# Performance work log

Hardware: AMD Instinct MI355X
Metric: run time of the kernel (lower is better)

Reference implementation:

```python
import jax, jax.numpy as jnp
import numpy as np

EMBED_DIM = 1024
NUM_HEADS = 16
HEAD_DIM = EMBED_DIM // NUM_HEADS
EXPANSION = 4
EPS = 1e-5


def setup_inputs() -> dict:
    key = jax.random.key(0)
    ks = jax.random.split(key, 8)
    D, F = EMBED_DIM, EMBED_DIM * EXPANSION
    s = lambda d: 1.0 / np.sqrt(d)
    return {
        "x": jax.random.normal(ks[0], (8, 1024, D), jnp.float32),
        "qkv_w": jax.random.normal(ks[1], (D, 3 * D), jnp.float32) * s(D),
        "qkv_b": jnp.zeros((3 * D,), jnp.float32),
        "out_w": jax.random.normal(ks[2], (D, D), jnp.float32) * s(D),
        "out_b": jnp.zeros((D,), jnp.float32),
        "ffn_w1": jax.random.normal(ks[3], (D, F), jnp.float32) * s(D),
        "ffn_b1": jnp.zeros((F,), jnp.float32),
        "ffn_w2": jax.random.normal(ks[4], (F, D), jnp.float32) * s(F),
        "ffn_b2": jnp.zeros((D,), jnp.float32),
        "ln1_g": jnp.ones((D,), jnp.float32),
        "ln1_b": jnp.zeros((D,), jnp.float32),
        "ln2_g": jnp.ones((D,), jnp.float32),
        "ln2_b": jnp.zeros((D,), jnp.float32),
    }


def _layernorm(x, g, b):
    mu = jnp.mean(x, axis=-1, keepdims=True)
    var = jnp.mean(jnp.square(x - mu), axis=-1, keepdims=True)
    return (x - mu) * jax.lax.rsqrt(var + EPS) * g + b


def reference(x, qkv_w, qkv_b, out_w, out_b, ffn_w1, ffn_b1, ffn_w2, ffn_b2,
              ln1_g, ln1_b, ln2_g, ln2_b):
    B, N, D = x.shape
    H, Hd = NUM_HEADS, HEAD_DIM
    scale = Hd ** -0.5

    residual = x
    h = _layernorm(x, ln1_g, ln1_b)
    qkv = h @ qkv_w + qkv_b                      # [B, N, 3D]
    q, k, v = jnp.split(qkv, 3, axis=-1)
    # [B, N, D] -> [B, H, N, Hd]
    reshape = lambda t: t.reshape(B, N, H, Hd).transpose(0, 2, 1, 3)
    q, k, v = reshape(q), reshape(k), reshape(v)

    attn = jnp.einsum("bhnd,bhmd->bhnm", q, k) * scale
    attn = jax.nn.softmax(attn, axis=-1)
    o = jnp.einsum("bhnm,bhmd->bhnd", attn, v)   # [B, H, N, Hd]
    o = o.transpose(0, 2, 1, 3).reshape(B, N, D)
    o = o @ out_w + out_b
    x = residual + o

    residual = x
    h = _layernorm(x, ln2_g, ln2_b)
    h = jax.nn.gelu(h @ ffn_w1 + ffn_b1, approximate=False) @ ffn_w2 + ffn_b2
    return residual + h
```

## Files before the change

kernel.cpp:

```cpp
#include <hip/hip_runtime.h>
#include <hip/hip_bf16.h>


typedef float f32x4 __attribute__((ext_vector_type(4)));
typedef float f32x16 __attribute__((ext_vector_type(16)));
typedef short bf16x8 __attribute__((ext_vector_type(8)));

#define DEV __device__ __forceinline__

DEV f32x4 mfma16(bf16x8 a, bf16x8 b, f32x4 c) {
    return __builtin_amdgcn_mfma_f32_16x16x32_bf16(a, b, c, 0, 0, 0);
}

DEV f32x16 mfma32(bf16x8 a, bf16x8 b, f32x16 c) {
    return __builtin_amdgcn_mfma_f32_32x32x16_bf16(a, b, c, 0, 0, 0);
}

DEV ushort f2bf(float f) {
    union { float f; unsigned u; } v; v.f = f;
    unsigned r = v.u + 0x7FFFu + ((v.u >> 16) & 1u);
    return (ushort)(r >> 16);
}

DEV unsigned cvtpk(float lo, float hi) {
    unsigned r;
    asm("v_cvt_pk_bf16_f32 %0, %1, %2" : "=v"(r) : "v"(lo), "v"(hi));
    return r;
}

DEV void gload_lds16(const void* g, void* l) {
    __builtin_amdgcn_global_load_lds(
        (const __attribute__((address_space(1))) void*)g,
        (__attribute__((address_space(3))) void*)l, 16, 0, 0);
}

template <int N> DEV void vmw() {
    if constexpr (N == 0)      asm volatile("s_waitcnt vmcnt(0)" ::: "memory");
    else if constexpr (N == 3) asm volatile("s_waitcnt vmcnt(3)" ::: "memory");
    else if constexpr (N == 4) asm volatile("s_waitcnt vmcnt(4)" ::: "memory");
    __builtin_amdgcn_sched_barrier(0);
}

#define SBAR() do { __builtin_amdgcn_sched_barrier(0); \
                    __builtin_amdgcn_s_barrier(); \
                    __builtin_amdgcn_sched_barrier(0); } while (0)
#define LGKM0() do { asm volatile("s_waitcnt lgkmcnt(0)" ::: "memory"); \
                     __builtin_amdgcn_sched_barrier(0); } while (0)

__global__ __launch_bounds__(256) void transpose_w(
    const float* __restrict__ src, ushort* __restrict__ dst, int K, int N)
{
    __shared__ float tile[32][33];
    const int n0 = blockIdx.x * 32, k0 = blockIdx.y * 32;
    const int tx = threadIdx.x, ty = threadIdx.y;
#pragma unroll
    for (int i = 0; i < 32; i += 8)
        tile[ty + i][tx] = src[(size_t)(k0 + ty + i) * N + n0 + tx];
    __syncthreads();
#pragma unroll
    for (int i = 0; i < 32; i += 8)
        dst[(size_t)(n0 + ty + i) * K + k0 + tx] = f2bf(tile[tx][ty + i]);
}

__global__ __launch_bounds__(256) void transpose_v(
    const ushort* __restrict__ qkvb, ushort* __restrict__ vt)
{
    __shared__ ushort tile[32][33];
    const int b = blockIdx.z >> 4, h = blockIdx.z & 15;
    const int n0 = blockIdx.x * 32, d0 = blockIdx.y * 32;
    const int tx = threadIdx.x, ty = threadIdx.y;
#pragma unroll
    for (int i = 0; i < 32; i += 8)
        tile[ty + i][tx] =
            qkvb[(size_t)(b * 1024 + n0 + ty + i) * 3072 + 2048 + h * 64 + d0 + tx];
    __syncthreads();
#pragma unroll
    for (int i = 0; i < 32; i += 8)
        vt[((size_t)(b * 16 + h) * 64 + d0 + ty + i) * 1024 + n0 + tx] = tile[tx][ty + i];
}

__global__ __launch_bounds__(256) void ln_bf16(
    const float* __restrict__ x, const float* __restrict__ gw,
    const float* __restrict__ bw, ushort* __restrict__ out)
{
    const int row = blockIdx.x;
    const int t = threadIdx.x;
    const float4 v = ((const float4*)(x + (size_t)row * 1024))[t];
    float s  = v.x + v.y + v.z + v.w;
    float s2 = v.x * v.x + v.y * v.y + v.z * v.z + v.w * v.w;
#pragma unroll
    for (int off = 32; off; off >>= 1) {
        s  += __shfl_xor(s, off);
        s2 += __shfl_xor(s2, off);
    }
    __shared__ float red[16];
    const int wave = t >> 6, lane = t & 63;
    if (lane == 0) { red[wave] = s; red[8 + wave] = s2; }
    __syncthreads();
    s  = red[0] + red[1] + red[2] + red[3];
    s2 = red[8] + red[9] + red[10] + red[11];
    const float mean = s * (1.0f / 1024.0f);
    const float var  = s2 * (1.0f / 1024.0f) - mean * mean;
    const float rstd = rsqrtf(var + 1e-5f);
    const float4 gv = ((const float4*)gw)[t];
    const float4 bv = ((const float4*)bw)[t];
    ushort4 o;
    o.x = f2bf((v.x - mean) * rstd * gv.x + bv.x);
    o.y = f2bf((v.y - mean) * rstd * gv.y + bv.y);
    o.z = f2bf((v.z - mean) * rstd * gv.z + bv.z);
    o.w = f2bf((v.w - mean) * rstd * gv.w + bv.w);
    ((ushort4*)out)[(size_t)row * 256 + t] = o;
}

template <int BM, int BN, int WM_, int WN_, int EPI>
__global__ __launch_bounds__(512, 2) void gemm8p(
    const ushort* __restrict__ A, const ushort* __restrict__ BT,
    const float* __restrict__ bias, const float* __restrict__ res,
    void* __restrict__ out, int M, int N, int K)
{
    constexpr int BK = 64;
    constexpr int MR = BM / WM_ / 16;
    constexpr int NR = BN / WN_ / 16;
    constexpr int MQ = MR / 2, NQ = NR / 2;
    constexpr int LA = (BM / 2) * BK * 2 / (512 * 16);
    constexpr int LB = (BN / 2) * BK * 2 / (512 * 16);
    constexpr int VMN = LA + LB;
    constexpr int ABYTES = BM * BK * 2;
    constexpr int BBYTES = BN * BK * 2;

    extern __shared__ __align__(16) char smem[];
#define ASB(buf) (smem + (buf) * ABYTES)
#define BSB(buf) (smem + 2 * ABYTES + (buf) * BBYTES)

    const int tid = threadIdx.x;
    const int wave = tid >> 6, lane = tid & 63;
    const int g = lane >> 4, lr = lane & 15;
    const int wr = wave / WN_, wc = wave % WN_;
    const int akey = (lr & 7) << 4;

    const int gx = gridDim.x;
    const int nwg = gx * gridDim.y;
    int id = blockIdx.y * gx + blockIdx.x;
    id = (id & 7) * (nwg >> 3) + (id >> 3);
    const int m0 = (id / gx) * BM, n0 = (id % gx) * BN;

    const int trow = tid >> 3;
    const int tblk = (tid & 7) ^ (trow & 7);
    const ushort* pA = A  + (size_t)(m0 + trow) * K + tblk * 8;
    const ushort* pB = BT + (size_t)(n0 + trow) * K + tblk * 8;
    const int woff = wave * 1024;

#define STAGE_A(buf, mh, kt) do { \
    _Pragma("unroll") for (int i = 0; i < LA; ++i) \
        gload_lds16(pA + ((size_t)((mh) * (BM / 2) + i * 64)) * K + (kt) * 64, \
                    ASB(buf) + (mh) * (BM / 2) * 128 + i * 8192 + woff); \
} while (0)
#define STAGE_B(buf, nh, kt) do { \
    _Pragma("unroll") for (int i = 0; i < LB; ++i) \
        gload_lds16(pB + ((size_t)((nh) * (BN / 2) + i * 64)) * K + (kt) * 64, \
                    BSB(buf) + (nh) * (BN / 2) * 128 + i * 8192 + woff); \
} while (0)

    bf16x8 af[MQ][2], bf[NR][2];
    f32x4 acc[MR][NR] = {};

#define LOAD_A(buf, mh) do { \
    const char* hb_ = ASB(buf) + (mh) * (BM / 2) * 128 + (wr * (MQ * 16) + lr) * 128; \
    _Pragma("unroll") for (int mt = 0; mt < MQ; ++mt) \
    _Pragma("unroll") for (int kk = 0; kk < 2; ++kk) \
        af[mt][kk] = *(const bf16x8*)(hb_ + mt * 2048 + ((kk * 64 + g * 16) ^ akey)); \
} while (0)
#define LOAD_B(buf, nh) do { \
    const char* hb_ = BSB(buf) + (nh) * (BN / 2) * 128 + (wc * (NQ * 16) + lr) * 128; \
    _Pragma("unroll") for (int nt = 0; nt < NQ; ++nt) \
    _Pragma("unroll") for (int kk = 0; kk < 2; ++kk) \
        bf[(nh) * NQ + nt][kk] = *(const bf16x8*)(hb_ + nt * 2048 + ((kk * 64 + g * 16) ^ akey)); \
} while (0)
#define MFMA_Q(MH, NH) do { \
    __builtin_amdgcn_s_setprio(1); \
    _Pragma("unroll") for (int mt = 0; mt < MQ; ++mt) \
    _Pragma("unroll") for (int nt = 0; nt < NQ; ++nt) \
    _Pragma("unroll") for (int kk = 0; kk < 2; ++kk) \
        acc[(MH) * MQ + mt][(NH) * NQ + nt] = \
            mfma16(af[mt][kk], bf[(NH) * NQ + nt][kk], acc[(MH) * MQ + mt][(NH) * NQ + nt]); \
    __builtin_amdgcn_s_setprio(0); \
} while (0)

    const int NT = K >> 6;

    STAGE_A(0, 0, 0); STAGE_B(0, 0, 0); STAGE_B(0, 1, 0); STAGE_A(0, 1, 0);
    STAGE_A(1, 0, 1); STAGE_B(1, 0, 1);
    vmw<VMN>();
    __builtin_amdgcn_s_barrier();

    for (int kt = 0; kt < NT; ++kt) {
        const int buf = kt & 1, nbuf = buf ^ 1;
        LOAD_A(buf, 0); LOAD_B(buf, 0);
        if (kt + 1 < NT) STAGE_B(nbuf, 1, kt + 1);
        SBAR(); LGKM0(); MFMA_Q(0, 0); SBAR();
        LOAD_B(buf, 1);
        if (kt + 1 < NT) STAGE_A(nbuf, 1, kt + 1);
        SBAR(); LGKM0(); MFMA_Q(0, 1); SBAR();
        LOAD_A(buf, 1);
        if (kt + 2 < NT) STAGE_A(buf, 0, kt + 2);
        SBAR(); LGKM0(); MFMA_Q(1, 1); SBAR();
        if (kt + 2 < NT) STAGE_B(buf, 0, kt + 2);
        SBAR(); LGKM0(); MFMA_Q(1, 0);
        if (kt + 2 < NT)      vmw<VMN>();
        else if (kt + 1 < NT) vmw<0>();
        SBAR();
    }

#pragma unroll
    for (int mi = 0; mi < MR; ++mi) {
        const int row0 = m0 + (mi / MQ) * (BM / 2) + wr * (MQ * 16) + (mi % MQ) * 16 + 4 * g;
#pragma unroll
        for (int ni = 0; ni < NR; ++ni) {
            const int col = n0 + (ni / NQ) * (BN / 2) + wc * (NQ * 16) + (ni % NQ) * 16 + lr;
            const float bv = bias[col];
#pragma unroll
            for (int r = 0; r < 4; ++r) {
                float v = acc[mi][ni][r] + bv;
                const size_t idx = (size_t)(row0 + r) * N + col;
                if constexpr (EPI == 1) {
                    ((float*)out)[idx] = v + res[idx];
                } else if constexpr (EPI == 2) {
                    v = 0.5f * v * (1.0f + erff(v * 0.70710678118654752f));
                    ((ushort*)out)[idx] = f2bf(v);
                } else {
                    ((ushort*)out)[idx] = f2bf(v);
                }
            }
        }
    }
#undef STAGE_A
#undef STAGE_B
#undef LOAD_A
#undef LOAD_B
#undef MFMA_Q
#undef ASB
#undef BSB
}

__global__ __launch_bounds__(256) void attn_kernel(
    const ushort* __restrict__ qkv, const ushort* __restrict__ vtb,
    ushort* __restrict__ o)
{
    __shared__ __align__(16) ushort Ks[64 * 64];
    __shared__ __align__(16) ushort Vt[64 * 64];

    const int tid = threadIdx.x;
    const int wave = tid >> 6, lane = tid & 63;
    const int lq = lane & 31;
    const int hi = lane >> 5;
    const int l7 = lane & 7;

    const int hwid = blockIdx.x;
    const int logical = (hwid & 7) * 128 + (hwid >> 3);
    const int bh = logical >> 3, qt = logical & 7;
    const int b = bh >> 4, head = bh & 15;
    const int q0 = qt * 128 + wave * 32;

    const size_t base  = (size_t)b * 1024 * 3072;
    const size_t vbase = (size_t)bh * 64 * 1024;

    union BF8 { bf16x8 v; ushort u[8]; unsigned w[4]; };

    BF8 qf[4];
    {
        const ushort* qrow = qkv + base + (size_t)(q0 + lq) * 3072 + head * 64;
#pragma unroll
        for (int s = 0; s < 4; ++s) {
            *(ushort4*)&qf[s].u[0] = *(const ushort4*)(qrow + 16 * s + 4 * hi);
            *(ushort4*)&qf[s].u[4] = *(const ushort4*)(qrow + 16 * s + 8 + 4 * hi);
        }
    }

    const int sr = tid >> 3, sc = tid & 7;
    const int swz = (sc ^ (sr & 7)) << 3;
    const ushort* kg0 = qkv + base + (size_t)sr * 3072 + 1024 + head * 64 + sc * 8;
    const ushort* kg1 = kg0 + (size_t)32 * 3072;
    const ushort* vg0 = vtb + vbase + (size_t)sr * 1024 + sc * 8;
    const ushort* vg1 = vg0 + (size_t)32 * 1024;
    ushort* ksw0 = Ks + sr * 64 + swz;
    ushort* ksw1 = Ks + (sr + 32) * 64 + swz;
    ushort* vsw0 = Vt + sr * 64 + swz;
    ushort* vsw1 = Vt + (sr + 32) * 64 + swz;

    float m_st = -1e30f, l_st = 0.f;
    f32x16 oacc[2] = {};

    constexpr float SCL = 0.18033688011112042f;

    for (int kt = 0; kt < 16; ++kt) {
        const int n0 = kt * 64;
        __syncthreads();
        *(bf16x8*)ksw0 = *(const bf16x8*)(kg0 + (size_t)n0 * 3072);
        *(bf16x8*)ksw1 = *(const bf16x8*)(kg1 + (size_t)n0 * 3072);
        *(bf16x8*)vsw0 = *(const bf16x8*)(vg0 + n0);
        *(bf16x8*)vsw1 = *(const bf16x8*)(vg1 + n0);
        __syncthreads();

        f32x16 sacc[2];
#pragma unroll
        for (int kb = 0; kb < 2; ++kb) {
            f32x16 a = {};
            const ushort* krow = Ks + (kb * 32 + lq) * 64;
#pragma unroll
            for (int s = 0; s < 4; ++s) {
                BF8 kf;
                *(ushort4*)&kf.u[0] = *(const ushort4*)(krow + (((2 * s)     ^ l7) << 3) + 4 * hi);
                *(ushort4*)&kf.u[4] = *(const ushort4*)(krow + (((2 * s + 1) ^ l7) << 3) + 4 * hi);
                a = mfma32(kf.v, qf[s].v, a);
            }
            sacc[kb] = a;
        }

        float mloc = -1e30f;
#pragma unroll
        for (int kb = 0; kb < 2; ++kb)
#pragma unroll
            for (int r = 0; r < 16; ++r)
                mloc = fmaxf(mloc, sacc[kb][r]);
        mloc = fmaxf(mloc, __shfl_xor(mloc, 32));
        const float mnew = fmaxf(m_st, mloc * SCL);
        const float resc = exp2f(m_st - mnew);
        m_st = mnew;

        float psum = 0.f;
#pragma unroll
        for (int kb = 0; kb < 2; ++kb)
#pragma unroll
            for (int r = 0; r < 16; ++r) {
                const float pe = exp2f(fmaf(sacc[kb][r], SCL, -mnew));
                sacc[kb][r] = pe;
                psum += pe;
            }
        psum += __shfl_xor(psum, 32);
        l_st = l_st * resc + psum;
#pragma unroll
        for (int nb = 0; nb < 2; ++nb)
#pragma unroll
            for (int r = 0; r < 16; ++r)
                oacc[nb][r] *= resc;

#pragma unroll
        for (int kb = 0; kb < 2; ++kb) {
            BF8 pf[2];
#pragma unroll
            for (int t = 0; t < 2; ++t)
#pragma unroll
                for (int w = 0; w < 4; ++w)
                    pf[t].w[w] = cvtpk(sacc[kb][8 * t + 2 * w], sacc[kb][8 * t + 2 * w + 1]);
#pragma unroll
            for (int nb = 0; nb < 2; ++nb) {
                const ushort* vrow = Vt + (nb * 32 + lq) * 64;
#pragma unroll
                for (int t = 0; t < 2; ++t) {
                    BF8 vf;
                    const int blk = 4 * kb + 2 * t;
                    *(ushort4*)&vf.u[0] = *(const ushort4*)(vrow + ((blk       ^ l7) << 3) + 4 * hi);
                    *(ushort4*)&vf.u[4] = *(const ushort4*)(vrow + (((blk + 1) ^ l7) << 3) + 4 * hi);
                    oacc[nb] = mfma32(vf.v, pf[t].v, oacc[nb]);
                }
            }
        }
    }

    const float inv = 1.0f / l_st;
    ushort* orow = o + (size_t)(b * 1024 + q0 + lq) * 1024 + head * 64;
#pragma unroll
    for (int nb = 0; nb < 2; ++nb)
#pragma unroll
        for (int u = 0; u < 4; ++u) {
            uint2 wv;
            wv.x = cvtpk(oacc[nb][4 * u] * inv,     oacc[nb][4 * u + 1] * inv);
            wv.y = cvtpk(oacc[nb][4 * u + 2] * inv, oacc[nb][4 * u + 3] * inv);
            *(uint2*)(orow + nb * 32 + 8 * u + 4 * hi) = wv;
        }
}

extern "C" void kernel_launch(void* const* d_in, const int* in_sizes, int n_in,
                              void* d_out, int out_size, void* d_ws, size_t ws_size,
                              hipStream_t stream)
{
    const float* x      = (const float*)d_in[0];
    const float* qkv_w  = (const float*)d_in[1];
    const float* qkv_b  = (const float*)d_in[2];
    const float* out_w  = (const float*)d_in[3];
    const float* out_b  = (const float*)d_in[4];
    const float* ffn_w1 = (const float*)d_in[5];
    const float* ffn_b1 = (const float*)d_in[6];
    const float* ffn_w2 = (const float*)d_in[7];
    const float* ffn_b2 = (const float*)d_in[8];
    const float* ln1_g  = (const float*)d_in[9];
    const float* ln1_b  = (const float*)d_in[10];
    const float* ln2_g  = (const float*)d_in[11];
    const float* ln2_b  = (const float*)d_in[12];

    constexpr size_t MB = 1u << 20;
    char* ws = (char*)d_ws;
    ushort* wt_qkv = (ushort*)(ws + 0 * MB);
    ushort* wt_out = (ushort*)(ws + 6 * MB);
    ushort* wt_f1  = (ushort*)(ws + 8 * MB);
    ushort* wt_f2  = (ushort*)(ws + 16 * MB);
    float*  x1     = (float*) (ws + 24 * MB);
    ushort* vtb    = (ushort*)(ws + 24 * MB);
    ushort* hbuf   = (ushort*)(ws + 56 * MB);
    ushort* qkvb   = (ushort*)(ws + 72 * MB);
    ushort* obuf   = (ushort*)(ws + 120 * MB);
    ushort* gbuf   = (ushort*)(ws + 72 * MB);

    const dim3 tb(32, 8);
    transpose_w<<<dim3(3072 / 32, 1024 / 32), tb, 0, stream>>>(qkv_w,  wt_qkv, 1024, 3072);
    transpose_w<<<dim3(1024 / 32, 1024 / 32), tb, 0, stream>>>(out_w,  wt_out, 1024, 1024);
    transpose_w<<<dim3(4096 / 32, 1024 / 32), tb, 0, stream>>>(ffn_w1, wt_f1,  1024, 4096);
    transpose_w<<<dim3(1024 / 32, 4096 / 32), tb, 0, stream>>>(ffn_w2, wt_f2,  4096, 1024);

    ln_bf16<<<8192, 256, 0, stream>>>(x, ln1_g, ln1_b, hbuf);

    constexpr int LDS_256 = (256 * 64 * 2 + 256 * 64 * 2) * 2;
    constexpr int LDS_128 = (256 * 64 * 2 + 128 * 64 * 2) * 2;

    gemm8p<256, 256, 2, 4, 0><<<dim3(12, 32), 512, LDS_256, stream>>>(
        hbuf, wt_qkv, qkv_b, nullptr, qkvb, 8192, 3072, 1024);

    transpose_v<<<dim3(32, 2, 128), tb, 0, stream>>>(qkvb, vtb);

    attn_kernel<<<1024, 256, 0, stream>>>(qkvb, vtb, obuf);

    gemm8p<256, 128, 4, 2, 1><<<dim3(8, 32), 512, LDS_128, stream>>>(
        obuf, wt_out, out_b, x, x1, 8192, 1024, 1024);

    ln_bf16<<<8192, 256, 0, stream>>>(x1, ln2_g, ln2_b, hbuf);

    gemm8p<256, 256, 2, 4, 2><<<dim3(16, 32), 512, LDS_256, stream>>>(
        hbuf, wt_f1, ffn_b1, nullptr, gbuf, 8192, 4096, 1024);

    gemm8p<256, 128, 4, 2, 1><<<dim3(8, 32), 512, LDS_128, stream>>>(
        gbuf, wt_f2, ffn_b2, x1, (float*)d_out, 8192, 1024, 4096);
}
```

Before: 388.4 us.

## Replace quadrant-interleaved GEMM schedule with register double-buffered fragment pipeline

Restructures the GEMM main loop to stage a whole K-tile per iteration and prefetch all A/B fragments for the next tile into a second register set while MFMAs run on the current one. This drops the four-phase quadrant schedule and its many barriers and sched_barriers in favour of two barriers per tile. It doubles fragment register usage, which risks spills or lower occupancy under the 512-thread, 2-block launch bound, and gives up the finer load/compute interleave.

```diff
diff --git a/kernel.cpp b/kernel.cpp
--- a/kernel.cpp
+++ b/kernel.cpp
@@ -34,18 +34,12 @@
         (__attribute__((address_space(3))) void*)l, 16, 0, 0);
 }
 
-template <int N> DEV void vmw() {
-    if constexpr (N == 0)      asm volatile("s_waitcnt vmcnt(0)" ::: "memory");
-    else if constexpr (N == 3) asm volatile("s_waitcnt vmcnt(3)" ::: "memory");
-    else if constexpr (N == 4) asm volatile("s_waitcnt vmcnt(4)" ::: "memory");
-    __builtin_amdgcn_sched_barrier(0);
-}
-
-#define SBAR() do { __builtin_amdgcn_sched_barrier(0); \
-                    __builtin_amdgcn_s_barrier(); \
-                    __builtin_amdgcn_sched_barrier(0); } while (0)
-#define LGKM0() do { asm volatile("s_waitcnt lgkmcnt(0)" ::: "memory"); \
-                     __builtin_amdgcn_sched_barrier(0); } while (0)
+template <int N> DEV void vmwait() {
+    asm volatile("s_waitcnt vmcnt(%0)" :: "n"(N) : "memory");
+}
+DEV void lgkm0() {
+    asm volatile("s_waitcnt lgkmcnt(0)" ::: "memory");
+}
 
 __global__ __launch_bounds__(256) void transpose_w(
     const float* __restrict__ src, ushort* __restrict__ dst, int K, int N)
@@ -113,7 +107,7 @@
 }
 
 template <int BM, int BN, int WM_, int WN_, int EPI>
-__global__ __launch_bounds__(512, 2) void gemm8p(
+__global__ __launch_bounds__(512, 2) void gemm_pipe(
     const ushort* __restrict__ A, const ushort* __restrict__ BT,
     const float* __restrict__ bias, const float* __restrict__ res,
     void* __restrict__ out, int M, int N, int K)
@@ -122,9 +116,7 @@
     constexpr int MR = BM / WM_ / 16;
     constexpr int NR = BN / WN_ / 16;
     constexpr int MQ = MR / 2, NQ = NR / 2;
-    constexpr int LA = (BM / 2) * BK * 2 / (512 * 16);
-    constexpr int LB = (BN / 2) * BK * 2 / (512 * 16);
-    constexpr int VMN = LA + LB;
+    constexpr int VT = (BM + BN) / 64;
     constexpr int ABYTES = BM * BK * 2;
     constexpr int BBYTES = BN * BK * 2;
 
@@ -150,65 +142,65 @@
     const ushort* pB = BT + (size_t)(n0 + trow) * K + tblk * 8;
     const int woff = wave * 1024;
 
-#define STAGE_A(buf, mh, kt) do { \
-    _Pragma("unroll") for (int i = 0; i < LA; ++i) \
-        gload_lds16(pA + ((size_t)((mh) * (BM / 2) + i * 64)) * K + (kt) * 64, \
-                    ASB(buf) + (mh) * (BM / 2) * 128 + i * 8192 + woff); \
+#define STAGE_TILE(buf, kt) do { \
+    _Pragma("unroll") for (int i = 0; i < BM / 64; ++i) \
+        gload_lds16(pA + ((size_t)(i * 64)) * K + (size_t)(kt) * 64, \
+                    ASB(buf) + i * 8192 + woff); \
+    _Pragma("unroll") for (int i = 0; i < BN / 64; ++i) \
+        gload_lds16(pB + ((size_t)(i * 64)) * K + (size_t)(kt) * 64, \
+                    BSB(buf) + i * 8192 + woff); \
 } while (0)
-#define STAGE_B(buf, nh, kt) do { \
-    _Pragma("unroll") for (int i = 0; i < LB; ++i) \
-        gload_lds16(pB + ((size_t)((nh) * (BN / 2) + i * 64)) * K + (kt) * 64, \
-                    BSB(buf) + (nh) * (BN / 2) * 128 + i * 8192 + woff); \
+
+    bf16x8 afE[MR][2], bfE[NR][2], afO[MR][2], bfO[NR][2];
+    f32x4 acc[MR][NR] = {};
+
+#define READ_FRAGS(AF, BF, buf) do { \
+    _Pragma("unroll") for (int mi = 0; mi < MR; ++mi) { \
+        const char* rb_ = ASB(buf) + (mi / MQ) * (BM / 2) * 128 \
+                        + (wr * (MQ * 16) + (mi % MQ) * 16 + lr) * 128; \
+        _Pragma("unroll") for (int kk = 0; kk < 2; ++kk) \
+            AF[mi][kk] = *(const bf16x8*)(rb_ + ((kk * 64 + g * 16) ^ akey)); \
+    } \
+    _Pragma("unroll") for (int ni = 0; ni < NR; ++ni) { \
+        const char* rb_ = BSB(buf) + (ni / NQ) * (BN / 2) * 128 \
+                        + (wc * (NQ * 16) + (ni % NQ) * 16 + lr) * 128; \
+        _Pragma("unroll") for (int kk = 0; kk < 2; ++kk) \
+            BF[ni][kk] = *(const bf16x8*)(rb_ + ((kk * 64 + g * 16) ^ akey)); \
+    } \
 } while (0)
 
-    bf16x8 af[MQ][2], bf[NR][2];
-    f32x4 acc[MR][NR] = {};
-
-#define LOAD_A(buf, mh) do { \
-    const char* hb_ = ASB(buf) + (mh) * (BM / 2) * 128 + (wr * (MQ * 16) + lr) * 128; \
-    _Pragma("unroll") for (int mt = 0; mt < MQ; ++mt) \
+#define MFMA_ALL(AF, BF) do { \
+    __builtin_amdgcn_s_setprio(1); \
+    _Pragma("unroll") for (int mi = 0; mi < MR; ++mi) \
+    _Pragma("unroll") for (int ni = 0; ni < NR; ++ni) \
     _Pragma("unroll") for (int kk = 0; kk < 2; ++kk) \
-        af[mt][kk] = *(const bf16x8*)(hb_ + mt * 2048 + ((kk * 64 + g * 16) ^ akey)); \
-} while (0)
-#define LOAD_B(buf, nh) do { \
-    const char* hb_ = BSB(buf) + (nh) * (BN / 2) * 128 + (wc * (NQ * 16) + lr) * 128; \
-    _Pragma("unroll") for (int nt = 0; nt < NQ; ++nt) \
-    _Pragma("unroll") for (int kk = 0; kk < 2; ++kk) \
-        bf[(nh) * NQ + nt][kk] = *(const bf16x8*)(hb_ + nt * 2048 + ((kk * 64 + g * 16) ^ akey)); \
-} while (0)
-#define MFMA_Q(MH, NH) do { \
-    __builtin_amdgcn_s_setprio(1); \
-    _Pragma("unroll") for (int mt = 0; mt < MQ; ++mt) \
-    _Pragma("unroll") for (int nt = 0; nt < NQ; ++nt) \
-    _Pragma("unroll") for (int kk = 0; kk < 2; ++kk) \
-        acc[(MH) * MQ + mt][(NH) * NQ + nt] = \
-            mfma16(af[mt][kk], bf[(NH) * NQ + nt][kk], acc[(MH) * MQ + mt][(NH) * NQ + nt]); \
+        acc[mi][ni] = mfma16(AF[mi][kk], BF[ni][kk], acc[mi][ni]); \
     __builtin_amdgcn_s_setprio(0); \
 } while (0)
 
+#define ITER(kt, CA, CB, PA, PB, BUFC) do { \
+    lgkm0();                                    \
+    __builtin_amdgcn_s_barrier();               \
+    if ((kt) + 2 < NT) STAGE_TILE(BUFC, (kt) + 2); \
+    if ((kt) + 1 < NT) { \
+        if ((kt) + 2 < NT) vmwait<VT>(); else vmwait<0>(); \
+        __builtin_amdgcn_s_barrier();           \
+        READ_FRAGS(PA, PB, 1 - (BUFC)); \
+    } \
+    MFMA_ALL(CA, CB); \
+} while (0)
+
     const int NT = K >> 6;
 
-    STAGE_A(0, 0, 0); STAGE_B(0, 0, 0); STAGE_B(0, 1, 0); STAGE_A(0, 1, 0);
-    STAGE_A(1, 0, 1); STAGE_B(1, 0, 1);
-    vmw<VMN>();
+    STAGE_TILE(0, 0);
+    STAGE_TILE(1, 1);
+    vmwait<VT>();
     __builtin_amdgcn_s_barrier();
-
-    for (int kt = 0; kt < NT; ++kt) {
-        const int buf = kt & 1, nbuf = buf ^ 1;
-        LOAD_A(buf, 0); LOAD_B(buf, 0);
-        if (kt + 1 < NT) STAGE_B(nbuf, 1, kt + 1);
-        SBAR(); LGKM0(); MFMA_Q(0, 0); SBAR();
-        LOAD_B(buf, 1);
-        if (kt + 1 < NT) STAGE_A(nbuf, 1, kt + 1);
-        SBAR(); LGKM0(); MFMA_Q(0, 1); SBAR();
-        LOAD_A(buf, 1);
-        if (kt + 2 < NT) STAGE_A(buf, 0, kt + 2);
-        SBAR(); LGKM0(); MFMA_Q(1, 1); SBAR();
-        if (kt + 2 < NT) STAGE_B(buf, 0, kt + 2);
-        SBAR(); LGKM0(); MFMA_Q(1, 0);
-        if (kt + 2 < NT)      vmw<VMN>();
-        else if (kt + 1 < NT) vmw<0>();
-        SBAR();
+    READ_FRAGS(afE, bfE, 0);
+
+    for (int kt = 0; kt < NT; kt += 2) {
+        ITER(kt,     afE, bfE, afO, bfO, 0);
+        ITER(kt + 1, afO, bfO, afE, bfE, 1);
     }
 
 #pragma unroll
@@ -233,11 +225,10 @@
             }
         }
     }
-#undef STAGE_A
-#undef STAGE_B
-#undef LOAD_A
-#undef LOAD_B
-#undef MFMA_Q
+#undef STAGE_TILE
+#undef READ_FRAGS
+#undef MFMA_ALL
+#undef ITER
 #undef ASB
 #undef BSB
 }
@@ -422,21 +413,21 @@
     constexpr int LDS_256 = (256 * 64 * 2 + 256 * 64 * 2) * 2;
     constexpr int LDS_128 = (256 * 64 * 2 + 128 * 64 * 2) * 2;
 
-    gemm8p<256, 256, 2, 4, 0><<<dim3(12, 32), 512, LDS_256, stream>>>(
+    gemm_pipe<256, 256, 2, 4, 0><<<dim3(12, 32), 512, LDS_256, stream>>>(
         hbuf, wt_qkv, qkv_b, nullptr, qkvb, 8192, 3072, 1024);
 
     transpose_v<<<dim3(32, 2, 128), tb, 0, stream>>>(qkvb, vtb);
 
     attn_kernel<<<1024, 256, 0, stream>>>(qkvb, vtb, obuf);
 
-    gemm8p<256, 128, 4, 2, 1><<<dim3(8, 32), 512, LDS_128, stream>>>(
+    gemm_pipe<256, 128, 4, 2, 1><<<dim3(8, 32), 512, LDS_128, stream>>>(
         obuf, wt_out, out_b, x, x1, 8192, 1024, 1024);
 
     ln_bf16<<<8192, 256, 0, stream>>>(x1, ln2_g, ln2_b, hbuf);
 
-    gemm8p<256, 256, 2, 4, 2><<<dim3(16, 32), 512, LDS_256, stream>>>(
+    gemm_pipe<256, 256, 2, 4, 2><<<dim3(16, 32), 512, LDS_256, stream>>>(
         hbuf, wt_f1, ffn_b1, nullptr, gbuf, 8192, 4096, 1024);
 
-    gemm8p<256, 128, 4, 2, 1><<<dim3(8, 32), 512, LDS_128, stream>>>(
+    gemm_pipe<256, 128, 4, 2, 1><<<dim3(8, 32), 512, LDS_128, stream>>>(
         gbuf, wt_f2, ffn_b2, x1, (float*)d_out, 8192, 1024, 4096);
 }
```

Result: slower. 985.4 us (+153.7%).
